# Kernel tuning notes

Measured on AMD Instinct MI355X. Metric: run time of the kernel, lower is better.

The kernel has to match this reference:

```python
import jax, jax.numpy as jnp
import numpy as np

NUM_HEAD = 16

def setup_inputs() -> dict:
    key = jax.random.key(0)
    ks = jax.random.split(key, 5)
    B, S, E = 2, 2048, 1024
    x = jax.random.normal(ks[0], (B, S, E), dtype=jnp.float32)
    w_qkv = jax.random.normal(ks[1], (3 * E, E), dtype=jnp.float32) * (E ** -0.5)
    b_qkv = jax.random.normal(ks[2], (3 * E,), dtype=jnp.float32) * 0.01
    w_out = jax.random.normal(ks[3], (E, E), dtype=jnp.float32) * (E ** -0.5)
    b_out = jax.random.normal(ks[4], (E,), dtype=jnp.float32) * 0.01
    return {"x": x, "w_qkv": w_qkv, "b_qkv": b_qkv, "w_out": w_out, "b_out": b_out}

def reference(x, w_qkv, b_qkv, w_out, b_out):
    B, S, E = x.shape
    H = NUM_HEAD
    D = E // H
    # fused QKV projection (torch Linear: x @ W^T + b)
    qkv = x @ w_qkv.T + b_qkv                       # [B, S, 3E]
    qkv = qkv.reshape(B, S, 3, H, D).transpose(2, 0, 3, 1, 4)  # [3, B, H, S, D]
    q, k, v = qkv[0], qkv[1], qkv[2]
    # NOTE: source scales by sqrt(embed_size), not sqrt(head_dim)
    scale = jnp.asarray(E, x.dtype) ** 0.5
    att = jnp.einsum('bhqd,bhkd->bhqk', q, k) / scale   # [B, H, S, S]
    # NOTE: source applies softmax over dim=1 (the head axis) — replicated faithfully
    att = jax.nn.softmax(att, axis=1)
    ctx = jnp.einsum('bhqk,bhkd->bhqd', att, v)         # [B, H, S, D]
    ctx = ctx.transpose(0, 2, 1, 3).reshape(B, S, E)    # [B, S, E]
    return ctx @ w_out.T + b_out
```

## Files before the change

### kernel.cpp

```cpp
#include <hip/hip_runtime.h>
#include <hip/hip_bf16.h>
#include <stdint.h>

typedef float  f32x4  __attribute__((ext_vector_type(4)));
typedef short  bf16x8 __attribute__((ext_vector_type(8)));
typedef short  bf16x4 __attribute__((ext_vector_type(4)));
typedef unsigned short u16x8 __attribute__((ext_vector_type(8)));

#define MFMA16(a, b, c) __builtin_amdgcn_mfma_f32_16x16x32_bf16((a), (b), (c), 0, 0, 0)

#if __has_builtin(__builtin_amdgcn_mfma_f32_16x16x16bf16_1k)
#define MFMA16K16(a, b, c) __builtin_amdgcn_mfma_f32_16x16x16bf16_1k((a), (b), (c), 0, 0, 0)
#else
__device__ __forceinline__ f32x4 mfma16k16_asm(bf16x4 a, bf16x4 b, f32x4 c) {
  f32x4 d;
  asm volatile("v_mfma_f32_16x16x16_bf16 %0, %1, %2, %3"
               : "=v"(d) : "v"(a), "v"(b), "v"(c));
  return d;
}
#define MFMA16K16(a, b, c) mfma16k16_asm((a), (b), (c))
#endif

__device__ __forceinline__ void gload16(const void* g, void* l) {
  __builtin_amdgcn_global_load_lds((const __attribute__((address_space(1))) void*)g,
                                   (__attribute__((address_space(3))) void*)l,
                                   16, 0, 0);
}

__device__ __forceinline__ unsigned short bf16bits(float f) {
  __hip_bfloat16 h = __float2bfloat16(f);
  return *(unsigned short*)&h;
}

__device__ __forceinline__ float bf2f(unsigned short u) {
  unsigned int x = ((unsigned int)u) << 16;
  return *(float*)&x;
}

__device__ __forceinline__ void block_sync_lds() {
  asm volatile("s_waitcnt lgkmcnt(0)" ::: "memory");
  __builtin_amdgcn_s_barrier();
  asm volatile("" ::: "memory");
}

__device__ __forceinline__ void fence_order() { asm volatile("" ::: "memory"); }

__global__ void cast_kernel(const float* __restrict__ s, __hip_bfloat16* __restrict__ d, int n4) {
  int i = blockIdx.x * blockDim.x + threadIdx.x;
  if (i < n4) {
    float4 v = ((const float4*)s)[i];
    ushort4 u;
    u.x = bf16bits(v.x); u.y = bf16bits(v.y); u.z = bf16bits(v.z); u.w = bf16bits(v.w);
    ((ushort4*)d)[i] = u;
  }
}

__global__ __launch_bounds__(256) void gemm_qkv_kernel(
    const __hip_bfloat16* __restrict__ A,
    const __hip_bfloat16* __restrict__ B,
    const float* __restrict__ bias,
    __hip_bfloat16* __restrict__ Qo,
    __hip_bfloat16* __restrict__ Ko,
    __hip_bfloat16* __restrict__ Vt) {
  const int K = 1024;
  __shared__ __align__(16) __hip_bfloat16 As[128 * 32];
  __shared__ __align__(16) __hip_bfloat16 Bs[128 * 32];
  const int t = threadIdx.x;
  const int lane = t & 63, wv = t >> 6;
  const int wm = (wv >> 1) * 64, wn = (wv & 1) * 64;
  const int lr = lane & 15, lq = lane >> 4;
  const int m0 = blockIdx.y * 128, n0 = blockIdx.x * 128;

  f32x4 acc[4][4] = {};

  const int arow = t >> 2;
  const int acol = (t & 3) * 8;
  const __hip_bfloat16* Ag = A + (long)(m0 + arow) * K + acol;
  const __hip_bfloat16* Bg = B + (long)(n0 + arow) * K + acol;
  __hip_bfloat16* Asl = As + t * 8;
  __hip_bfloat16* Bsl = Bs + t * 8;

  for (int kk = 0; kk < K; kk += 32) {
    gload16(Ag + kk, Asl);
    gload16(Ag + kk + 64 * K, Asl + 2048);
    gload16(Bg + kk, Bsl);
    gload16(Bg + kk + 64 * K, Bsl + 2048);
    __syncthreads();
    bf16x8 af[4], bf[4];
#pragma unroll
    for (int i = 0; i < 4; ++i)
      af[i] = *(const bf16x8*)&As[(wm + i * 16 + lr) * 32 + lq * 8];
#pragma unroll
    for (int j = 0; j < 4; ++j)
      bf[j] = *(const bf16x8*)&Bs[(wn + j * 16 + lr) * 32 + lq * 8];
#pragma unroll
    for (int i = 0; i < 4; ++i)
#pragma unroll
      for (int j = 0; j < 4; ++j)
        acc[i][j] = MFMA16(af[i], bf[j], acc[i][j]);
    __syncthreads();
  }

#pragma unroll
  for (int i = 0; i < 4; ++i) {
#pragma unroll
    for (int j = 0; j < 4; ++j) {
      int col = n0 + wn + j * 16 + lr;
      int tsel = col >> 10, rem = col & 1023;
      int h = rem >> 6, d = rem & 63;
      float bs = bias[col];
      int rowb = m0 + wm + i * 16 + lq * 4;
#pragma unroll
      for (int r = 0; r < 4; ++r) {
        int m = rowb + r;
        int b = m >> 11, sdx = m & 2047;
        __hip_bfloat16 v = __float2bfloat16(acc[i][j][r] + bs);
        long bh = (long)(b * 16 + h);
        if (tsel == 0)       Qo[(bh * 2048 + sdx) * 64 + d] = v;
        else if (tsel == 1)  Ko[(bh * 2048 + sdx) * 64 + d] = v;
        else                 Vt[(bh * 64 + d) * 2048 + sdx] = v;
      }
    }
  }
}

__global__ __launch_bounds__(512, 2) void attn_kernel(
    const __hip_bfloat16* __restrict__ Q,
    const __hip_bfloat16* __restrict__ K,
    const __hip_bfloat16* __restrict__ Vt,
    __hip_bfloat16* __restrict__ part) {
  __shared__ __align__(16) __hip_bfloat16 KsA[16 * 16 * 64];
  __shared__ __align__(16) __hip_bfloat16 KsB[16 * 16 * 64];
  __shared__ __align__(16) __hip_bfloat16 VsA[16 * 64 * 16];
  __shared__ __align__(16) __hip_bfloat16 VsB[16 * 64 * 16];
  __shared__ __align__(16) float psum[2 * 8 * 16 * 16];

  const int t = threadIdx.x, lane = t & 63, wv = t >> 6;
  const int lr = lane & 15, lq = lane >> 4;
  const int h0 = wv * 2;
  const int combo = blockIdx.x & 7;
  const int b = combo & 1, chunk = combo >> 1;
  const int q0 = (blockIdx.x >> 3) * 32;
  const int k0 = chunk * 512;
  const float c = 0.03125f * 1.44269504f;
  const long bh16 = (long)(b * 16);

  auto stageK = [&](__hip_bfloat16* dst, int kks) {
#pragma unroll
    for (int cc = 0; cc < 4; ++cc) {
      const int p = cc * 8192 + t * 16;
      const int rho = p >> 7;
      const int hh = rho >> 4, kl = rho & 15;
      const int g = ((p >> 4) & 7) ^ (rho & 7);
      const __hip_bfloat16* src = K + ((bh16 + hh) * 2048 + kks + kl) * 64 + g * 8;
      gload16(src, (char*)dst + p);
    }
    fence_order();
  };
  auto stageV = [&](__hip_bfloat16* dst, int kks) {
#pragma unroll
    for (int cc = 0; cc < 4; ++cc) {
      const int p = cc * 8192 + t * 16;
      const int rho = p >> 5;
      const int hh = rho >> 6, d = rho & 63;
      const int g = (p >> 4) & 1;
      const __hip_bfloat16* src = Vt + ((bh16 + hh) * 64 + d) * 2048 + kks + g * 8;
      gload16(src, (char*)dst + p);
    }
    fence_order();
  };

  bf16x8 qf[2][2][2];
#pragma unroll
  for (int hh = 0; hh < 2; ++hh)
#pragma unroll
    for (int qt = 0; qt < 2; ++qt)
#pragma unroll
      for (int dh = 0; dh < 2; ++dh)
        qf[hh][qt][dh] = *(const bf16x8*)(
            Q + ((bh16 + h0 + hh) * 2048 + q0 + qt * 16 + lr) * 64 + dh * 32 + lq * 8);

  stageK(KsA, k0);
  stageV(VsA, k0);
  asm volatile("s_waitcnt vmcnt(0)" ::: "memory");
  block_sync_lds();

  f32x4 ctx[2][2][4] = {};

  auto body = [&](const __hip_bfloat16* Kc, const __hip_bfloat16* Vc,
                  __hip_bfloat16* Kn, __hip_bfloat16* Vn, int kt) {
    if (kt < 31) {
      stageK(Kn, k0 + (kt + 1) * 16);
      stageV(Vn, k0 + (kt + 1) * 16);
    }
    f32x4 s[2][2];
    __builtin_amdgcn_s_setprio(1);
#pragma unroll
    for (int hh = 0; hh < 2; ++hh) {
      const int rho = (h0 + hh) * 16 + lr;
      const __hip_bfloat16* kr = Kc + rho * 64;
      bf16x8 kf0 = *(const bf16x8*)(kr + ((lq ^ (rho & 7)) << 3));
      bf16x8 kf1 = *(const bf16x8*)(kr + (((lq + 4) ^ (rho & 7)) << 3));
#pragma unroll
      for (int qt = 0; qt < 2; ++qt) {
        f32x4 a = {};
        a = MFMA16(kf0, qf[hh][qt][0], a);
        a = MFMA16(kf1, qf[hh][qt][1], a);
        s[hh][qt] = a;
      }
    }
    __builtin_amdgcn_s_setprio(0);
#pragma unroll
    for (int qt = 0; qt < 2; ++qt) {
      f32x4 pp;
#pragma unroll
      for (int r = 0; r < 4; ++r) {
        s[0][qt][r] = __builtin_amdgcn_exp2f(s[0][qt][r] * c);
        s[1][qt][r] = __builtin_amdgcn_exp2f(s[1][qt][r] * c);
        pp[r] = s[0][qt][r] + s[1][qt][r];
      }
      *(f32x4*)&psum[qt * 2048 + wv * 256 + lr * 16 + lq * 4] = pp;
    }
    block_sync_lds();
    if (wv < 2) {
      f32x4 tot = {};
#pragma unroll
      for (int w2 = 0; w2 < 8; ++w2)
        tot += *(const f32x4*)&psum[wv * 2048 + w2 * 256 + lr * 16 + lq * 4];
      f32x4 inv;
#pragma unroll
      for (int r = 0; r < 4; ++r) inv[r] = __builtin_amdgcn_rcpf(tot[r]);
      *(f32x4*)&psum[wv * 2048 + lr * 16 + lq * 4] = inv;
    }
    block_sync_lds();
    __builtin_amdgcn_s_setprio(1);
    f32x4 inv0 = *(const f32x4*)&psum[lr * 16 + lq * 4];
    f32x4 inv1 = *(const f32x4*)&psum[2048 + lr * 16 + lq * 4];
#pragma unroll
    for (int hh = 0; hh < 2; ++hh) {
      const char* vb = (const char*)Vc + (h0 + hh) * 2048;
      bf16x4 vf[4];
#pragma unroll
      for (int dt = 0; dt < 4; ++dt)
        vf[dt] = *(const bf16x4*)(vb + (dt * 16 + lr) * 32 + lq * 8);
#pragma unroll
      for (int qt = 0; qt < 2; ++qt) {
        const f32x4 iv = qt ? inv1 : inv0;
        bf16x4 p4;
#pragma unroll
        for (int r = 0; r < 4; ++r) p4[r] = (short)bf16bits(s[hh][qt][r] * iv[r]);
#pragma unroll
        for (int dt = 0; dt < 4; ++dt)
          ctx[hh][qt][dt] = MFMA16K16(vf[dt], p4, ctx[hh][qt][dt]);
      }
    }
    __builtin_amdgcn_s_setprio(0);
    asm volatile("s_waitcnt vmcnt(0)" ::: "memory");
    block_sync_lds();
  };

#pragma unroll 1
  for (int kp = 0; kp < 16; ++kp) {
    body(KsA, VsA, KsB, VsB, 2 * kp);
    body(KsB, VsB, KsA, VsA, 2 * kp + 1);
  }

  unsigned short* Pc = (unsigned short*)KsA;
#pragma unroll
  for (int qt = 0; qt < 2; ++qt) {
    if (qt) block_sync_lds();
#pragma unroll
    for (int hh = 0; hh < 2; ++hh) {
      const int h = h0 + hh;
#pragma unroll
      for (int dt = 0; dt < 4; ++dt) {
        bf16x4 pk;
#pragma unroll
        for (int r = 0; r < 4; ++r) pk[r] = (short)bf16bits(ctx[hh][qt][dt][r]);
        const int o = h * 128 + dt * 32 + lq * 8;
        *(bf16x4*)((char*)Pc + lr * 2048 + (o ^ ((lr & 7) << 4))) = pk;
      }
    }
    block_sync_lds();
    unsigned short* gbase = (unsigned short*)part +
        ((long)(chunk * 4096 + b * 2048 + q0 + qt * 16)) * 1024;
#pragma unroll
    for (int j = 0; j < 4; ++j) {
      int gf = (j * 512 + t) * 8;
      int q = gf >> 10, hd = gf & 1023;
      u16x8 v = *(const u16x8*)((char*)Pc + q * 2048 + ((hd * 2) ^ ((q & 7) << 4)));
      *(u16x8*)&gbase[gf] = v;
    }
  }
}

__global__ void reduce_cast_kernel(const unsigned short* __restrict__ part,
                                   __hip_bfloat16* __restrict__ dst) {
  int i = blockIdx.x * blockDim.x + threadIdx.x;
  const long S4 = (long)4096 * 1024 / 4;
  const ushort4* p = (const ushort4*)part;
  float sx = 0.f, sy = 0.f, sz = 0.f, sw = 0.f;
#pragma unroll
  for (int c = 0; c < 4; ++c) {
    ushort4 v = p[i + c * S4];
    sx += bf2f(v.x); sy += bf2f(v.y); sz += bf2f(v.z); sw += bf2f(v.w);
  }
  ushort4 u;
  u.x = bf16bits(sx); u.y = bf16bits(sy); u.z = bf16bits(sz); u.w = bf16bits(sw);
  ((ushort4*)dst)[i] = u;
}

__global__ __launch_bounds__(256) void gemm_out_kernel(
    const __hip_bfloat16* __restrict__ A,
    const __hip_bfloat16* __restrict__ B,
    const float* __restrict__ bias,
    float* __restrict__ out) {
  const int K = 1024;
  __shared__ __align__(16) __hip_bfloat16 As[128 * 32];
  __shared__ __align__(16) __hip_bfloat16 Bs[128 * 32];
  const int t = threadIdx.x;
  const int lane = t & 63, wv = t >> 6;
  const int wm = (wv >> 1) * 64, wn = (wv & 1) * 64;
  const int lr = lane & 15, lq = lane >> 4;
  const int m0 = blockIdx.y * 128, n0 = blockIdx.x * 128;

  f32x4 acc[4][4] = {};

  const int arow = t >> 2;
  const int acol = (t & 3) * 8;
  const __hip_bfloat16* Ag = A + (long)(m0 + arow) * K + acol;
  const __hip_bfloat16* Bg = B + (long)(n0 + arow) * K + acol;
  __hip_bfloat16* Asl = As + t * 8;
  __hip_bfloat16* Bsl = Bs + t * 8;

  for (int kk = 0; kk < K; kk += 32) {
    gload16(Ag + kk, Asl);
    gload16(Ag + kk + 64 * K, Asl + 2048);
    gload16(Bg + kk, Bsl);
    gload16(Bg + kk + 64 * K, Bsl + 2048);
    __syncthreads();
    bf16x8 af[4], bf[4];
#pragma unroll
    for (int i = 0; i < 4; ++i)
      af[i] = *(const bf16x8*)&As[(wm + i * 16 + lr) * 32 + lq * 8];
#pragma unroll
    for (int j = 0; j < 4; ++j)
      bf[j] = *(const bf16x8*)&Bs[(wn + j * 16 + lr) * 32 + lq * 8];
#pragma unroll
    for (int i = 0; i < 4; ++i)
#pragma unroll
      for (int j = 0; j < 4; ++j)
        acc[i][j] = MFMA16(af[i], bf[j], acc[i][j]);
    __syncthreads();
  }

#pragma unroll
  for (int i = 0; i < 4; ++i) {
#pragma unroll
    for (int j = 0; j < 4; ++j) {
      int col = n0 + wn + j * 16 + lr;
      float bs = bias[col];
      int rowb = m0 + wm + i * 16 + lq * 4;
#pragma unroll
      for (int r = 0; r < 4; ++r) {
        out[(long)(rowb + r) * 1024 + col] = acc[i][j][r] + bs;
      }
    }
  }
}

extern "C" void kernel_launch(void* const* d_in, const int* in_sizes, int n_in,
                              void* d_out, int out_size, void* d_ws, size_t ws_size,
                              hipStream_t stream) {
  const float* x     = (const float*)d_in[0];
  const float* w_qkv = (const float*)d_in[1];
  const float* b_qkv = (const float*)d_in[2];
  const float* w_out = (const float*)d_in[3];
  const float* b_out = (const float*)d_in[4];
  float* out = (float*)d_out;
  char* ws = (char*)d_ws;

  __hip_bfloat16* xb    = (__hip_bfloat16*)(ws);
  __hip_bfloat16* wqkvb = (__hip_bfloat16*)(ws + (8ul << 20));
  __hip_bfloat16* woutb = (__hip_bfloat16*)(ws + (14ul << 20));
  __hip_bfloat16* Qb    = (__hip_bfloat16*)(ws + (16ul << 20));
  __hip_bfloat16* Kb    = (__hip_bfloat16*)(ws + (24ul << 20));
  __hip_bfloat16* Vtb   = (__hip_bfloat16*)(ws + (32ul << 20));
  __hip_bfloat16* partb = (__hip_bfloat16*)(ws + (40ul << 20));
  __hip_bfloat16* ctxb  = (__hip_bfloat16*)(ws + (72ul << 20));

  cast_kernel<<<4096, 256, 0, stream>>>(x, xb, 4194304 / 4);
  cast_kernel<<<3072, 256, 0, stream>>>(w_qkv, wqkvb, 3145728 / 4);
  cast_kernel<<<1024, 256, 0, stream>>>(w_out, woutb, 1048576 / 4);
  gemm_qkv_kernel<<<dim3(24, 32), 256, 0, stream>>>(xb, wqkvb, b_qkv, Qb, Kb, Vtb);
  attn_kernel<<<512, 512, 0, stream>>>(Qb, Kb, Vtb, partb);
  reduce_cast_kernel<<<4096, 256, 0, stream>>>((const unsigned short*)partb, ctxb);
  gemm_out_kernel<<<dim3(8, 32), 256, 0, stream>>>(ctxb, woutb, b_out, out);
}
```

Before: 320.8 us.

## Load V fragments directly from global, drop V LDS staging, raise occupancy

Result: slower. 492.7 us (+53.6%).

```diff
diff --git a/kernel.cpp b/kernel.cpp
--- a/kernel.cpp
+++ b/kernel.cpp
@@ -124,15 +124,13 @@
   }
 }
 
-__global__ __launch_bounds__(512, 2) void attn_kernel(
+__global__ __launch_bounds__(512, 4) void attn_kernel(
     const __hip_bfloat16* __restrict__ Q,
     const __hip_bfloat16* __restrict__ K,
     const __hip_bfloat16* __restrict__ Vt,
     __hip_bfloat16* __restrict__ part) {
   __shared__ __align__(16) __hip_bfloat16 KsA[16 * 16 * 64];
   __shared__ __align__(16) __hip_bfloat16 KsB[16 * 16 * 64];
-  __shared__ __align__(16) __hip_bfloat16 VsA[16 * 64 * 16];
-  __shared__ __align__(16) __hip_bfloat16 VsB[16 * 64 * 16];
   __shared__ __align__(16) float psum[2 * 8 * 16 * 16];
 
   const int t = threadIdx.x, lane = t & 63, wv = t >> 6;
@@ -144,6 +142,7 @@
   const int k0 = chunk * 512;
   const float c = 0.03125f * 1.44269504f;
   const long bh16 = (long)(b * 16);
+  const int rot = ((lq + lr) & 3) * 4;
 
   auto stageK = [&](__hip_bfloat16* dst, int kks) {
 #pragma unroll
@@ -157,18 +156,6 @@
     }
     fence_order();
   };
-  auto stageV = [&](__hip_bfloat16* dst, int kks) {
-#pragma unroll
-    for (int cc = 0; cc < 4; ++cc) {
-      const int p = cc * 8192 + t * 16;
-      const int rho = p >> 5;
-      const int hh = rho >> 6, d = rho & 63;
-      const int g = (p >> 4) & 1;
-      const __hip_bfloat16* src = Vt + ((bh16 + hh) * 64 + d) * 2048 + kks + g * 8;
-      gload16(src, (char*)dst + p);
-    }
-    fence_order();
-  };
 
   bf16x8 qf[2][2][2];
 #pragma unroll
@@ -181,18 +168,22 @@
             Q + ((bh16 + h0 + hh) * 2048 + q0 + qt * 16 + lr) * 64 + dh * 32 + lq * 8);
 
   stageK(KsA, k0);
-  stageV(VsA, k0);
   asm volatile("s_waitcnt vmcnt(0)" ::: "memory");
   block_sync_lds();
 
   f32x4 ctx[2][2][4] = {};
 
-  auto body = [&](const __hip_bfloat16* Kc, const __hip_bfloat16* Vc,
-                  __hip_bfloat16* Kn, __hip_bfloat16* Vn, int kt) {
-    if (kt < 31) {
-      stageK(Kn, k0 + (kt + 1) * 16);
-      stageV(Vn, k0 + (kt + 1) * 16);
-    }
+  auto body = [&](const __hip_bfloat16* Kc, __hip_bfloat16* Kn, int kt) {
+    const int kk = k0 + kt * 16;
+    bf16x4 vg[2][4];
+#pragma unroll
+    for (int hh = 0; hh < 2; ++hh) {
+      const __hip_bfloat16* vb = Vt + ((bh16 + h0 + hh) * 64 + lr) * 2048 + kk + lq * 4;
+#pragma unroll
+      for (int dt = 0; dt < 4; ++dt)
+        vg[hh][dt] = *(const bf16x4*)(vb + (long)dt * 16 * 2048);
+    }
+    if (kt < 31) stageK(Kn, kk + 16);
     f32x4 s[2][2];
     __builtin_amdgcn_s_setprio(1);
 #pragma unroll
@@ -219,30 +210,26 @@
         s[1][qt][r] = __builtin_amdgcn_exp2f(s[1][qt][r] * c);
         pp[r] = s[0][qt][r] + s[1][qt][r];
       }
-      *(f32x4*)&psum[qt * 2048 + wv * 256 + lr * 16 + lq * 4] = pp;
+      *(f32x4*)&psum[qt * 2048 + wv * 256 + lr * 16 + rot] = pp;
     }
     block_sync_lds();
     if (wv < 2) {
       f32x4 tot = {};
 #pragma unroll
       for (int w2 = 0; w2 < 8; ++w2)
-        tot += *(const f32x4*)&psum[wv * 2048 + w2 * 256 + lr * 16 + lq * 4];
+        tot += *(const f32x4*)&psum[wv * 2048 + w2 * 256 + lr * 16 + rot];
       f32x4 inv;
 #pragma unroll
       for (int r = 0; r < 4; ++r) inv[r] = __builtin_amdgcn_rcpf(tot[r]);
-      *(f32x4*)&psum[wv * 2048 + lr * 16 + lq * 4] = inv;
-    }
+      *(f32x4*)&psum[wv * 2048 + lr * 16 + rot] = inv;
+    }
+    asm volatile("s_waitcnt vmcnt(0)" ::: "memory");
     block_sync_lds();
     __builtin_amdgcn_s_setprio(1);
-    f32x4 inv0 = *(const f32x4*)&psum[lr * 16 + lq * 4];
-    f32x4 inv1 = *(const f32x4*)&psum[2048 + lr * 16 + lq * 4];
+    f32x4 inv0 = *(const f32x4*)&psum[lr * 16 + rot];
+    f32x4 inv1 = *(const f32x4*)&psum[2048 + lr * 16 + rot];
 #pragma unroll
     for (int hh = 0; hh < 2; ++hh) {
-      const char* vb = (const char*)Vc + (h0 + hh) * 2048;
-      bf16x4 vf[4];
-#pragma unroll
-      for (int dt = 0; dt < 4; ++dt)
-        vf[dt] = *(const bf16x4*)(vb + (dt * 16 + lr) * 32 + lq * 8);
 #pragma unroll
       for (int qt = 0; qt < 2; ++qt) {
         const f32x4 iv = qt ? inv1 : inv0;
@@ -251,18 +238,16 @@
         for (int r = 0; r < 4; ++r) p4[r] = (short)bf16bits(s[hh][qt][r] * iv[r]);
 #pragma unroll
         for (int dt = 0; dt < 4; ++dt)
-          ctx[hh][qt][dt] = MFMA16K16(vf[dt], p4, ctx[hh][qt][dt]);
+          ctx[hh][qt][dt] = MFMA16K16(vg[hh][dt], p4, ctx[hh][qt][dt]);
       }
     }
     __builtin_amdgcn_s_setprio(0);
-    asm volatile("s_waitcnt vmcnt(0)" ::: "memory");
-    block_sync_lds();
   };
 
 #pragma unroll 1
   for (int kp = 0; kp < 16; ++kp) {
-    body(KsA, VsA, KsB, VsB, 2 * kp);
-    body(KsB, VsB, KsA, VsA, 2 * kp + 1);
+    body(KsA, KsB, 2 * kp);
+    body(KsB, KsA, 2 * kp + 1);
   }
 
   unsigned short* Pc = (unsigned short*)KsA;
```
